# Kernel tuning notes

Hardware: AMD Instinct MI355X
Metric: run time of the kernel (lower is better)

## Reference

```python
import jax, jax.numpy as jnp
import numpy as np

EMBED_DIM = 400
HEAD_SIZE = 64


def setup_inputs() -> dict:
    key = jax.random.key(0)
    k1, k2, k3, k4 = jax.random.split(key, 4)
    B, T, C = 8, 2048, EMBED_DIM
    x = jax.random.normal(k1, (B, T, C), dtype=jnp.float32)
    # Linear(embed_dim, head_size, bias=False) weights, stored as [C, H] for x @ W
    s = 1.0 / np.sqrt(C)
    Wq = jax.random.uniform(k2, (C, HEAD_SIZE), dtype=jnp.float32, minval=-s, maxval=s)
    Wk = jax.random.uniform(k3, (C, HEAD_SIZE), dtype=jnp.float32, minval=-s, maxval=s)
    Wv = jax.random.uniform(k4, (C, HEAD_SIZE), dtype=jnp.float32, minval=-s, maxval=s)
    return {"x": x, "Wq": Wq, "Wk": Wk, "Wv": Wv}


def reference(x, Wq, Wk, Wv):
    B, T, C = x.shape
    q = x @ Wq  # [B,T,H]
    k = x @ Wk  # [B,T,H]
    v = x @ Wv  # [B,T,H]
    scale = 1.0 / jnp.sqrt(jnp.asarray(q.shape[-1], q.dtype))
    scores = jnp.einsum('bth,bsh->bts', q, k) * scale  # [B,T,T]
    causal = jnp.tril(jnp.ones((T, T), dtype=bool))
    scores = jnp.where(causal, scores, jnp.asarray(-jnp.inf, scores.dtype))
    attn = jax.nn.softmax(scores, axis=-1)
    out = jnp.einsum('bts,bsh->bth', attn, v)  # [B,T,H]
    return out
```

## Files before the change

kernel.cpp:

```cpp
#include <hip/hip_runtime.h>
#include <math.h>

#define B_SZ   8
#define T_SEQ  2048
#define C_DIM  400
#define H_DIM  64
#define NROWS  (B_SZ * T_SEQ)
#define QT_TILES (T_SEQ / 64)
#define LDSTR  424
#define NCH    8
#define TPC    4
#define NKS    13

typedef short s8v  __attribute__((ext_vector_type(8)));
typedef float f32x4 __attribute__((ext_vector_type(4)));
typedef unsigned u32x4 __attribute__((ext_vector_type(4)));

__device__ __forceinline__ unsigned short f2bf(float f) {
    unsigned int u = __float_as_uint(f);
    u = (u + 0x7FFFu + ((u >> 16) & 1u)) >> 16;
    return (unsigned short)u;
}

__device__ __forceinline__ float bf2f(unsigned short u) {
    return __uint_as_float((unsigned)u << 16);
}

__device__ __forceinline__ unsigned cvtpk_bf16(float lo, float hi) {
    unsigned r;
    asm("v_cvt_pk_bf16_f32 %0, %1, %2" : "=v"(r) : "v"(lo), "v"(hi));
    return r;
}

__global__ __launch_bounds__(256) void wprep_kernel(
    const float* __restrict__ Wq, const float* __restrict__ Wk,
    const float* __restrict__ Wv, unsigned short* __restrict__ WtP)
{
    int idx = blockIdx.x * 256 + threadIdx.x;
    int j    = idx & 7;
    int lane = (idx >> 3) & 63;
    int fks  = idx >> 9;
    int f    = fks / NKS;
    int ks   = fks - f * NKS;
    int m    = f >> 2;
    int col  = (f & 3) * 16 + (lane & 15);
    int k    = ks * 32 + (lane >> 4) * 8 + j;
    const float* W = (m == 0) ? Wq : (m == 1) ? Wk : Wv;
    float v = (k < C_DIM) ? W[k * H_DIM + col] : 0.0f;
    if (m == 0) v *= 0.125f * 1.44269504088896f;
    WtP[idx] = f2bf(v);
}

__global__ __launch_bounds__(256) void proj_kernel(
    const float* __restrict__ x, const unsigned short* __restrict__ WtP,
    unsigned short* __restrict__ Qb, unsigned short* __restrict__ Kb,
    unsigned short* __restrict__ Vt)
{
    __shared__ unsigned short xl[32 * LDSTR];
    const int tid = threadIdx.x;
    const int tile = blockIdx.x;

    const float4* __restrict__ x4 = (const float4*)x;
    for (int idx = tid; idx < 32 * 104; idx += 256) {
        int row = idx / 104, c4 = idx - row * 104;
        ushort4 wv;
        if (c4 < 100) {
            float4 v = x4[(size_t)(tile * 32 + row) * 100 + c4];
            wv.x = f2bf(v.x); wv.y = f2bf(v.y); wv.z = f2bf(v.z); wv.w = f2bf(v.w);
        } else { wv.x = wv.y = wv.z = wv.w = 0; }
        *(ushort4*)&xl[row * LDSTR + c4 * 4] = wv;
    }
    __syncthreads();

    const int w = tid >> 6, l = tid & 63;
    const int lr = l & 15, g = l >> 4;

    f32x4 acc[3][2];
#pragma unroll
    for (int fl = 0; fl < 3; ++fl)
#pragma unroll
        for (int rg = 0; rg < 2; ++rg) acc[fl][rg] = (f32x4)0.f;

    const char* const Wp = (const char*)WtP;
    for (int ks = 0; ks < NKS; ++ks) {
        s8v a0 = *(const s8v*)&xl[lr        * LDSTR + ks * 32 + g * 8];
        s8v a1 = *(const s8v*)&xl[(16 + lr) * LDSTR + ks * 32 + g * 8];
#pragma unroll
        for (int fl = 0; fl < 3; ++fl) {
            int f = w * 3 + fl;
            const s8v b = *(const s8v*)(Wp + ((f * NKS + ks) << 10) + (l << 4));
            acc[fl][0] = __builtin_amdgcn_mfma_f32_16x16x32_bf16(a0, b, acc[fl][0], 0, 0, 0);
            acc[fl][1] = __builtin_amdgcn_mfma_f32_16x16x32_bf16(a1, b, acc[fl][1], 0, 0, 0);
        }
    }

#pragma unroll
    for (int fl = 0; fl < 3; ++fl) {
        int f = w * 3 + fl;
        int m = f >> 2, col = (f & 3) * 16 + lr;
#pragma unroll
        for (int rg = 0; rg < 2; ++rg)
#pragma unroll
            for (int r = 0; r < 4; ++r) {
                int row_g = tile * 32 + rg * 16 + g * 4 + r;
                unsigned short bv = f2bf(acc[fl][rg][r]);
                if (m == 0)      Qb[(size_t)row_g * H_DIM + col] = bv;
                else if (m == 1) Kb[(size_t)row_g * H_DIM + col] = bv;
                else {
                    int b = row_g >> 11, t = row_g & 2047;
                    Vt[((size_t)b * H_DIM + col) * T_SEQ + t] = bv;
                }
            }
    }
}

__global__ __launch_bounds__(256) void attn_kernel(
    const unsigned short* __restrict__ Qb, const unsigned short* __restrict__ Kb,
    const unsigned short* __restrict__ Vt,
    unsigned short* __restrict__ Opart, float* __restrict__ lpart)
{
    const int c  = blockIdx.x;
    const int qt = blockIdx.y;
    const int b  = blockIdx.z;
    if (c * TPC > qt) return;
    const int kt0 = c * TPC;
    const int kend = min(kt0 + (TPC - 1), qt);

    __shared__ char smem[2][16384];

    const int tid = threadIdx.x;
    const int w = tid >> 6, l = tid & 63;
    const int lr = l & 15, g = l >> 4;
    const int q0 = qt * 64 + w * 16;

    const int r0 = tid >> 3;
    const int ch = tid & 7;
    const int swz = (ch * 16) ^ ((r0 & 7) << 4);
    const char* const Kg = (const char*)(Kb + (size_t)b * T_SEQ * H_DIM);
    const char* const Vg = (const char*)(Vt + (size_t)b * H_DIM * T_SEQ);

    uint4 kA, kB, vA, vB;
    auto LD = [&](int kt) {
        kA = *(const uint4*)(Kg + (size_t)(kt * 64 + r0     ) * 128 + ch * 16);
        kB = *(const uint4*)(Kg + (size_t)(kt * 64 + r0 + 32) * 128 + ch * 16);
        vA = *(const uint4*)(Vg + (size_t)(r0     ) * 4096 + kt * 128 + ch * 16);
        vB = *(const uint4*)(Vg + (size_t)(r0 + 32) * 4096 + kt * 128 + ch * 16);
    };
    auto ST = [&](int buf) {
        char* Kl = smem[buf];
        char* Vl = smem[buf] + 8192;
        *(uint4*)(Kl + r0 * 128 + swz)        = kA;
        *(uint4*)(Kl + (r0 + 32) * 128 + swz) = kB;
        *(uint4*)(Vl + r0 * 128 + swz)        = vA;
        *(uint4*)(Vl + (r0 + 32) * 128 + swz) = vB;
    };

    s8v aq[2];
#pragma unroll
    for (int s = 0; s < 2; ++s)
        aq[s] = *(const s8v*)&Qb[((size_t)b * T_SEQ + q0 + lr) * H_DIM + s * 32 + g * 8];

    f32x4 acc[4];
#pragma unroll
    for (int f = 0; f < 4; ++f) acc[f] = (f32x4)0.f;
    float lsum = 0.f;

    LD(kt0); ST(0);
    if (kt0 < kend) LD(kt0 + 1);
    __syncthreads();
    int cur = 0;

    for (int kt = kt0; kt <= kend; ++kt) {
        char* const Kl = smem[cur];
        char* const Vl = smem[cur] + 8192;

        f32x4 sacc[4];
#pragma unroll
        for (int f = 0; f < 4; ++f) sacc[f] = (f32x4)0.f;
        __builtin_amdgcn_s_setprio(1);
#pragma unroll
        for (int f = 0; f < 4; ++f)
#pragma unroll
            for (int s = 0; s < 2; ++s) {
                const s8v ak = *(const s8v*)(Kl + (f * 16 + lr) * 128
                                             + (((s * 4 + g) * 16) ^ ((lr & 7) << 4)));
                sacc[f] = __builtin_amdgcn_mfma_f32_16x16x32_bf16(ak, aq[s], sacc[f], 0, 0, 0);
            }
        __builtin_amdgcn_s_setprio(0);

        float p[4][4];
        if (kt == qt) {
            const int q_my = q0 + lr;
#pragma unroll
            for (int f = 0; f < 4; ++f)
#pragma unroll
                for (int r = 0; r < 4; ++r) {
                    float pv = __builtin_amdgcn_exp2f(sacc[f][r]);
                    p[f][r] = ((kt * 64 + f * 16 + g * 4 + r) > q_my) ? 0.0f : pv;
                }
        } else {
#pragma unroll
            for (int f = 0; f < 4; ++f)
#pragma unroll
                for (int r = 0; r < 4; ++r)
                    p[f][r] = __builtin_amdgcn_exp2f(sacc[f][r]);
        }
#pragma unroll
        for (int f = 0; f < 4; ++f)
            lsum += (p[f][0] + p[f][1]) + (p[f][2] + p[f][3]);

        s8v ap[2];
#pragma unroll
        for (int s = 0; s < 2; ++s) {
            unsigned Fa = cvtpk_bf16(p[2 * s][0],     p[2 * s][1]);
            unsigned Fb = cvtpk_bf16(p[2 * s][2],     p[2 * s][3]);
            unsigned Ga = cvtpk_bf16(p[2 * s + 1][0], p[2 * s + 1][1]);
            unsigned Gb = cvtpk_bf16(p[2 * s + 1][2], p[2 * s + 1][3]);
            asm("v_permlane32_swap_b32 %0, %1" : "+v"(Fa), "+v"(Ga));
            asm("v_permlane16_swap_b32 %0, %1" : "+v"(Fa), "+v"(Ga));
            asm("v_permlane32_swap_b32 %0, %1" : "+v"(Fb), "+v"(Gb));
            asm("v_permlane16_swap_b32 %0, %1" : "+v"(Fb), "+v"(Gb));
            u32x4 wv; wv.x = Fa; wv.y = Fb; wv.z = Ga; wv.w = Gb;
            ap[s] = __builtin_bit_cast(s8v, wv);
        }

        __builtin_amdgcn_s_setprio(1);
#pragma unroll
        for (int f = 0; f < 4; ++f)
#pragma unroll
            for (int s = 0; s < 2; ++s) {
                const s8v bv = *(const s8v*)(Vl + (f * 16 + lr) * 128
                                             + (((s * 4 + g) * 16) ^ ((lr & 7) << 4)));
                acc[f] = __builtin_amdgcn_mfma_f32_16x16x32_bf16(ap[s], bv, acc[f], 0, 0, 0);
            }
        __builtin_amdgcn_s_setprio(0);

        if (kt < kend) {
            ST(cur ^ 1);
            if (kt + 1 < kend) LD(kt + 2);
            __syncthreads();
            cur ^= 1;
        }
    }

    lsum += __shfl_xor(lsum, 16, 64);
    lsum += __shfl_xor(lsum, 32, 64);

    const size_t pb = ((size_t)(b * QT_TILES + qt) * NCH + c);
    unsigned short* const Op = Opart + pb * 4096;
#pragma unroll
    for (int f = 0; f < 4; ++f)
#pragma unroll
        for (int r = 0; r < 4; ++r)
            Op[(w * 16 + g * 4 + r) * 64 + f * 16 + lr] = f2bf(acc[f][r]);
    if (l < 16)
        lpart[pb * 64 + w * 16 + l] = lsum;
}

__global__ __launch_bounds__(256) void combine_kernel(
    const unsigned short* __restrict__ Opart, const float* __restrict__ lpart,
    float* __restrict__ out)
{
    const int idx = blockIdx.x * 256 + threadIdx.x;
    const int row = idx >> 4, h4 = idx & 15;
    const int b = row >> 11, t = row & 2047;
    const int qt = t >> 6, r = t & 63;
    const int nch = (qt >> 2) + 1;

    float4 os = make_float4(0.f, 0.f, 0.f, 0.f);
    float ls = 0.f;
    const size_t base = (size_t)(b * QT_TILES + qt) * NCH;
    for (int cc = 0; cc < nch; ++cc) {
        ushort4 v = *(const ushort4*)&Opart[(base + cc) * 4096 + r * 64 + h4 * 4];
        os.x += bf2f(v.x); os.y += bf2f(v.y); os.z += bf2f(v.z); os.w += bf2f(v.w);
        ls += lpart[(base + cc) * 64 + r];
    }
    float inv = 1.0f / ls;
    ((float4*)out)[idx] = make_float4(os.x * inv, os.y * inv, os.z * inv, os.w * inv);
}

extern "C" void kernel_launch(void* const* d_in, const int* in_sizes, int n_in,
                              void* d_out, int out_size, void* d_ws, size_t ws_size,
                              hipStream_t stream)
{
    const float* x  = (const float*)d_in[0];
    const float* Wq = (const float*)d_in[1];
    const float* Wk = (const float*)d_in[2];
    const float* Wv = (const float*)d_in[3];
    float* out = (float*)d_out;

    char* ws = (char*)d_ws;
    unsigned short* WtP = (unsigned short*)(ws);
    unsigned short* Qb = (unsigned short*)(ws + 163840);
    unsigned short* Kb = (unsigned short*)(ws + 163840 + 2097152);
    unsigned short* Vt = (unsigned short*)(ws + 163840 + 2 * 2097152);
    unsigned short* Opart = (unsigned short*)(ws + 163840 + 3 * 2097152);
    float* lpart = (float*)(ws + 163840 + 3 * 2097152 + 16777216);

    wprep_kernel<<<(12 * NKS * 512) / 256, 256, 0, stream>>>(Wq, Wk, Wv, WtP);
    proj_kernel<<<NROWS / 32, 256, 0, stream>>>(x, WtP, Qb, Kb, Vt);
    attn_kernel<<<dim3(NCH, QT_TILES, B_SZ), 256, 0, stream>>>(Qb, Kb, Vt, Opart, lpart);
    combine_kernel<<<(NROWS * H_DIM / 4) / 256, 256, 0, stream>>>(Opart, lpart, out);
}
```

Baseline: 43.77 us.

## Pre-pack K and V in MFMA fragment layout, load directly from global in attention

The projection kernel now stages K and V tiles in LDS and writes them to global memory already arranged in per-lane MFMA operand order. The attention kernel then loads K and V fragments straight from global into registers, with no LDS double buffering and no block-wide barriers. This removes LDS traffic and synchronisation from the attention loop. In exchange it relies on global/L2 latency being hidden without an explicit prefetch stage, and it adds a redundant zero store before each packed K write.

```diff
diff --git a/kernel.cpp b/kernel.cpp
--- a/kernel.cpp
+++ b/kernel.cpp
@@ -37,6 +37,7 @@
     const float* __restrict__ Wv, unsigned short* __restrict__ WtP)
 {
     int idx = blockIdx.x * 256 + threadIdx.x;
+    if (idx >= 12 * NKS * 512) return;
     int j    = idx & 7;
     int lane = (idx >> 3) & 63;
     int fks  = idx >> 9;
@@ -53,10 +54,12 @@
 
 __global__ __launch_bounds__(256) void proj_kernel(
     const float* __restrict__ x, const unsigned short* __restrict__ WtP,
-    unsigned short* __restrict__ Qb, unsigned short* __restrict__ Kb,
-    unsigned short* __restrict__ Vt)
+    unsigned short* __restrict__ Qb, unsigned short* __restrict__ KbP,
+    unsigned short* __restrict__ VtP)
 {
     __shared__ unsigned short xl[32 * LDSTR];
+    __shared__ unsigned short Klds[32 * 72];
+    __shared__ unsigned short Vlds[64 * 40];
     const int tid = threadIdx.x;
     const int tile = blockIdx.x;
 
@@ -98,25 +101,55 @@
     for (int fl = 0; fl < 3; ++fl) {
         int f = w * 3 + fl;
         int m = f >> 2, col = (f & 3) * 16 + lr;
-#pragma unroll
-        for (int rg = 0; rg < 2; ++rg)
-#pragma unroll
-            for (int r = 0; r < 4; ++r) {
-                int row_g = tile * 32 + rg * 16 + g * 4 + r;
-                unsigned short bv = f2bf(acc[fl][rg][r]);
-                if (m == 0)      Qb[(size_t)row_g * H_DIM + col] = bv;
-                else if (m == 1) Kb[(size_t)row_g * H_DIM + col] = bv;
-                else {
-                    int b = row_g >> 11, t = row_g & 2047;
-                    Vt[((size_t)b * H_DIM + col) * T_SEQ + t] = bv;
-                }
+        if (m == 0) {
+#pragma unroll
+            for (int rg = 0; rg < 2; ++rg)
+#pragma unroll
+                for (int r = 0; r < 4; ++r)
+                    Qb[(size_t)(tile * 32 + rg * 16 + g * 4 + r) * H_DIM + col]
+                        = f2bf(acc[fl][rg][r]);
+        } else if (m == 1) {
+#pragma unroll
+            for (int rg = 0; rg < 2; ++rg)
+#pragma unroll
+                for (int r = 0; r < 4; ++r)
+                    Klds[(rg * 16 + g * 4 + r) * 72 + col] = f2bf(acc[fl][rg][r]);
+        } else {
+#pragma unroll
+            for (int rg = 0; rg < 2; ++rg) {
+                ushort4 pk;
+                pk.x = f2bf(acc[fl][rg][0]); pk.y = f2bf(acc[fl][rg][1]);
+                pk.z = f2bf(acc[fl][rg][2]); pk.w = f2bf(acc[fl][rg][3]);
+                *(ushort4*)&Vlds[col * 40 + rg * 16 + g * 4] = pk;
             }
+        }
+    }
+    __syncthreads();
+
+    const int bb   = tile >> 6;
+    const int kt   = (tile & 63) >> 1;
+    const int half = tile & 1;
+    for (int idx2 = tid; idx2 < 512; idx2 += 256) {
+        int fr = idx2 >> 6, lane = idx2 & 63;
+        if (fr < 4) {
+            int fi = fr >> 1, s = fr & 1;
+            s8v v = *(const s8v*)&Klds[(fi * 16 + (lane & 15)) * 72
+                                       + s * 32 + (lane >> 4) * 8];
+            int f = half * 2 + fi;
+            KbP[((((size_t)bb * 32 + kt) * 4 + f) * 2 + s) * 512 + lane * 8] = 0;
+            *(s8v*)&KbP[((((size_t)bb * 32 + kt) * 4 + f) * 2 + s) * 512 + lane * 8] = v;
+        } else {
+            int fh = fr - 4;
+            s8v v = *(const s8v*)&Vlds[(fh * 16 + (lane & 15)) * 40
+                                       + (lane >> 4) * 8];
+            *(s8v*)&VtP[((((size_t)bb * 32 + kt) * 4 + fh) * 2 + half) * 512 + lane * 8] = v;
+        }
     }
 }
 
 __global__ __launch_bounds__(256) void attn_kernel(
-    const unsigned short* __restrict__ Qb, const unsigned short* __restrict__ Kb,
-    const unsigned short* __restrict__ Vt,
+    const unsigned short* __restrict__ Qb, const unsigned short* __restrict__ KbP,
+    const unsigned short* __restrict__ VtP,
     unsigned short* __restrict__ Opart, float* __restrict__ lpart)
 {
     const int c  = blockIdx.x;
@@ -126,34 +159,13 @@
     const int kt0 = c * TPC;
     const int kend = min(kt0 + (TPC - 1), qt);
 
-    __shared__ char smem[2][16384];
-
     const int tid = threadIdx.x;
     const int w = tid >> 6, l = tid & 63;
     const int lr = l & 15, g = l >> 4;
     const int q0 = qt * 64 + w * 16;
 
-    const int r0 = tid >> 3;
-    const int ch = tid & 7;
-    const int swz = (ch * 16) ^ ((r0 & 7) << 4);
-    const char* const Kg = (const char*)(Kb + (size_t)b * T_SEQ * H_DIM);
-    const char* const Vg = (const char*)(Vt + (size_t)b * H_DIM * T_SEQ);
-
-    uint4 kA, kB, vA, vB;
-    auto LD = [&](int kt) {
-        kA = *(const uint4*)(Kg + (size_t)(kt * 64 + r0     ) * 128 + ch * 16);
-        kB = *(const uint4*)(Kg + (size_t)(kt * 64 + r0 + 32) * 128 + ch * 16);
-        vA = *(const uint4*)(Vg + (size_t)(r0     ) * 4096 + kt * 128 + ch * 16);
-        vB = *(const uint4*)(Vg + (size_t)(r0 + 32) * 4096 + kt * 128 + ch * 16);
-    };
-    auto ST = [&](int buf) {
-        char* Kl = smem[buf];
-        char* Vl = smem[buf] + 8192;
-        *(uint4*)(Kl + r0 * 128 + swz)        = kA;
-        *(uint4*)(Kl + (r0 + 32) * 128 + swz) = kB;
-        *(uint4*)(Vl + r0 * 128 + swz)        = vA;
-        *(uint4*)(Vl + (r0 + 32) * 128 + swz) = vB;
-    };
+    const char* const Kp = (const char*)(KbP + (size_t)b * 32 * 4096) + l * 16;
+    const char* const Vp = (const char*)(VtP + (size_t)b * 32 * 4096) + l * 16;
 
     s8v aq[2];
 #pragma unroll
@@ -165,14 +177,16 @@
     for (int f = 0; f < 4; ++f) acc[f] = (f32x4)0.f;
     float lsum = 0.f;
 
-    LD(kt0); ST(0);
-    if (kt0 < kend) LD(kt0 + 1);
-    __syncthreads();
-    int cur = 0;
-
     for (int kt = kt0; kt <= kend; ++kt) {
-        char* const Kl = smem[cur];
-        char* const Vl = smem[cur] + 8192;
+        const char* const Kt = Kp + (size_t)kt * 8192;
+        const char* const Vt2 = Vp + (size_t)kt * 8192;
+
+        s8v bk[4][2];
+#pragma unroll
+        for (int f = 0; f < 4; ++f)
+#pragma unroll
+            for (int s = 0; s < 2; ++s)
+                bk[f][s] = *(const s8v*)(Kt + (f * 2 + s) * 1024);
 
         f32x4 sacc[4];
 #pragma unroll
@@ -181,12 +195,16 @@
 #pragma unroll
         for (int f = 0; f < 4; ++f)
 #pragma unroll
-            for (int s = 0; s < 2; ++s) {
-                const s8v ak = *(const s8v*)(Kl + (f * 16 + lr) * 128
-                                             + (((s * 4 + g) * 16) ^ ((lr & 7) << 4)));
-                sacc[f] = __builtin_amdgcn_mfma_f32_16x16x32_bf16(ak, aq[s], sacc[f], 0, 0, 0);
-            }
+            for (int s = 0; s < 2; ++s)
+                sacc[f] = __builtin_amdgcn_mfma_f32_16x16x32_bf16(bk[f][s], aq[s], sacc[f], 0, 0, 0);
         __builtin_amdgcn_s_setprio(0);
+
+        s8v bv[4][2];
+#pragma unroll
+        for (int f = 0; f < 4; ++f)
+#pragma unroll
+            for (int s = 0; s < 2; ++s)
+                bv[f][s] = *(const s8v*)(Vt2 + (f * 2 + s) * 1024);
 
         float p[4][4];
         if (kt == qt) {
@@ -228,19 +246,9 @@
 #pragma unroll
         for (int f = 0; f < 4; ++f)
 #pragma unroll
-            for (int s = 0; s < 2; ++s) {
-                const s8v bv = *(const s8v*)(Vl + (f * 16 + lr) * 128
-                                             + (((s * 4 + g) * 16) ^ ((lr & 7) << 4)));
-                acc[f] = __builtin_amdgcn_mfma_f32_16x16x32_bf16(ap[s], bv, acc[f], 0, 0, 0);
-            }
+            for (int s = 0; s < 2; ++s)
+                acc[f] = __builtin_amdgcn_mfma_f32_16x16x32_bf16(ap[s], bv[f][s], acc[f], 0, 0, 0);
         __builtin_amdgcn_s_setprio(0);
-
-        if (kt < kend) {
-            ST(cur ^ 1);
-            if (kt + 1 < kend) LD(kt + 2);
-            __syncthreads();
-            cur ^= 1;
-        }
     }
 
     lsum += __shfl_xor(lsum, 16, 64);
@@ -291,14 +299,14 @@
 
     char* ws = (char*)d_ws;
     unsigned short* WtP = (unsigned short*)(ws);
-    unsigned short* Qb = (unsigned short*)(ws + 163840);
-    unsigned short* Kb = (unsigned short*)(ws + 163840 + 2097152);
-    unsigned short* Vt = (unsigned short*)(ws + 163840 + 2 * 2097152);
+    unsigned short* Qb  = (unsigned short*)(ws + 163840);
+    unsigned short* KbP = (unsigned short*)(ws + 163840 + 2097152);
+    unsigned short* VtP = (unsigned short*)(ws + 163840 + 2 * 2097152);
     unsigned short* Opart = (unsigned short*)(ws + 163840 + 3 * 2097152);
     float* lpart = (float*)(ws + 163840 + 3 * 2097152 + 16777216);
 
-    wprep_kernel<<<(12 * NKS * 512) / 256, 256, 0, stream>>>(Wq, Wk, Wv, WtP);
-    proj_kernel<<<NROWS / 32, 256, 0, stream>>>(x, WtP, Qb, Kb, Vt);
-    attn_kernel<<<dim3(NCH, QT_TILES, B_SZ), 256, 0, stream>>>(Qb, Kb, Vt, Opart, lpart);
+    wprep_kernel<<<(12 * NKS * 512 + 255) / 256, 256, 0, stream>>>(Wq, Wk, Wv, WtP);
+    proj_kernel<<<NROWS / 32, 256, 0, stream>>>(x, WtP, Qb, KbP, VtP);
+    attn_kernel<<<dim3(NCH, QT_TILES, B_SZ), 256, 0, stream>>>(Qb, KbP, VtP, Opart, lpart);
     combine_kernel<<<(NROWS * H_DIM / 4) / 256, 256, 0, stream>>>(Opart, lpart, out);
 }
```

Result: slower. 48.16 us (+10.0%).
